# Optimization experiments

Measured on AMD Instinct MI355X. Metric: run time of the kernel, lower is better.

## Reference

```python
import jax, jax.numpy as jnp
import numpy as np

B, AT, NBR = 8, 96, 512
NG, NT = 25, 5            # n_gaussian_triple, n_theta
NANG = NG * NT            # 125, filternet input dim
NF = 128                  # n_filters
NB = 128                  # n_atom_basis


def ssp(x):
    # shifted softplus: ln(0.5*e^x + 0.5) = softplus(x) - ln(2)
    return jax.nn.softplus(x) - jnp.asarray(np.log(2.0), x.dtype)


def setup_inputs() -> dict:
    key = jax.random.key(0)
    ks = jax.random.split(key, 16)
    s = lambda fan_in: 1.0 / np.sqrt(fan_in)
    return {
        "x": jax.random.normal(ks[0], (B, AT, NB), jnp.float32),
        "triple_ijk": jax.random.uniform(ks[1], (B, AT, NBR, NANG), jnp.float32),
        "neighbors_j": jax.random.randint(ks[2], (B, AT, NBR), 0, AT, jnp.int32),
        "neighbors_k": jax.random.randint(ks[3], (B, AT, NBR), 0, AT, jnp.int32),
        "triple_mask": jnp.ones((B, AT, NBR), jnp.float32),
        # filter network (Dense ssp -> Dense linear)
        "W1": jax.random.normal(ks[4], (NANG, NF), jnp.float32) * s(NANG),
        "b1": jnp.zeros((NF,), jnp.float32),
        "W2": jax.random.normal(ks[5], (NF, NF), jnp.float32) * s(NF),
        "b2": jnp.zeros((NF,), jnp.float32),
        # cfconv in2f (no bias) and f2out (ssp activation)
        "Win": jax.random.normal(ks[6], (NB, NF), jnp.float32) * s(NB),
        "Wf2": jax.random.normal(ks[7], (NF, NB), jnp.float32) * s(NF),
        "bf2": jnp.zeros((NB,), jnp.float32),
        # final dense (linear) before residual
        "Wd": jax.random.normal(ks[8], (NB, NB), jnp.float32) * s(NB),
        "bd": jnp.zeros((NB,), jnp.float32),
    }


def _gather_atoms(y, nbh):
    # y: (B, At, F); nbh: (B, At, Nbr) -> (B, At, Nbr, F)
    b, at, nbr = nbh.shape
    idx = nbh.reshape(b, at * nbr, 1)
    return jnp.take_along_axis(y, idx, axis=1).reshape(b, at, nbr, y.shape[-1])


def reference(x, triple_ijk, neighbors_j, neighbors_k, triple_mask,
              W1, b1, W2, b2, Win, Wf2, bf2, Wd, bd):
    # filter network on angular/radial triple features -> (B, At, Nbr, NF)
    W_triple = ssp(triple_ijk @ W1 + b1) @ W2 + b2
    # in2f
    y = x @ Win                                  # (B, At, NF)
    y_j = _gather_atoms(y, neighbors_j)          # (B, At, Nbr, NF)
    y_k = _gather_atoms(y, neighbors_k)          # (B, At, Nbr, NF)
    # element-wise continuous-filter conv over triples, mask padded triples
    yt = y_j * y_k * W_triple * triple_mask[..., None]
    agg = jnp.sum(yt, axis=2)                    # sum-aggregate over triples
    v = ssp(agg @ Wf2 + bf2)                     # f2out with shifted softplus
    v = v @ Wd + bd                              # interaction dense
    return x + v                                 # residual
```

## Files before the change

### kernel.cpp

```cpp
#include <hip/hip_runtime.h>
#include <math.h>

#define B_    8
#define AT_   96
#define NBR_  512
#define NANG_ 125
#define NF_   128
#define NB_   128
#define TN    32
#define NCHUNK 2
#define CROWS (NBR_ / NCHUNK)
#define NTI   (CROWS / TN)
#define YSTB  40

typedef __attribute__((ext_vector_type(8))) short bf16x8;
typedef __attribute__((ext_vector_type(4))) float f32x4;
typedef __attribute__((ext_vector_type(4))) unsigned u32x4;

__device__ __forceinline__ short f2bf(float f) {
    union { float f; unsigned u; } x; x.f = f;
    return (short)((x.u + 0x8000u) >> 16);
}

__device__ __forceinline__ float bf2f(unsigned short u) {
    union { unsigned u; float f; } x; x.u = ((unsigned)u) << 16;
    return x.f;
}

__device__ __forceinline__ float sspf(float x) {
    float p = __builtin_amdgcn_exp2f(x * 1.44269504088896340736f);
    float l = __builtin_amdgcn_logf(1.0f + p);
    return 0.69314718055994530942f * l - 0.69314718055994530942f;
}

__device__ __forceinline__ unsigned cvtpk(float lo, float hi) {
    unsigned r;
    asm("v_cvt_pk_bf16_f32 %0, %1, %2" : "=v"(r) : "v"(lo), "v"(hi));
    return r;
}

__device__ __forceinline__ void block_sync_lds() {
    asm volatile("s_waitcnt lgkmcnt(0)" ::: "memory");
    __builtin_amdgcn_s_barrier();
    __builtin_amdgcn_sched_barrier(0);
}

__device__ __forceinline__ void load_tile(const float* __restrict__ tile,
                                          int row, int seg, float* v) {
    const float* s = tile + row * NANG_ + seg * 16;
    if (seg < 7) {
        #pragma unroll
        for (int j = 0; j < 16; j++) v[j] = s[j];
    } else {
        #pragma unroll
        for (int j = 0; j < 13; j++) v[j] = s[j];
        v[13] = 0.f; v[14] = 0.f; v[15] = 0.f;
    }
}

__device__ __forceinline__ void store_swz(short* dst, int row, int seg, const float* v) {
    unsigned r[8];
    #pragma unroll
    for (int i = 0; i < 8; i++) r[i] = cvtpk(v[2 * i], v[2 * i + 1]);
    const int swz = (row & 7) << 4;
    char* base = (char*)dst + row * 256;
    *(u32x4*)(base + ((seg * 32) ^ swz))      = (u32x4){r[0], r[1], r[2], r[3]};
    *(u32x4*)(base + ((seg * 32 + 16) ^ swz)) = (u32x4){r[4], r[5], r[6], r[7]};
}

__global__ __launch_bounds__(128) void prep_kernel(
    const float* __restrict__ x, const float* __restrict__ Win,
    const float* __restrict__ W1, const float* __restrict__ W2,
    float* __restrict__ y, short* __restrict__ w1p, short* __restrict__ w2p)
{
    __shared__ float xs[4][NB_];
    int blk = blockIdx.x, tid = threadIdx.x;
    if (blk < 192) {
        int row0 = blk * 4;
        #pragma unroll
        for (int r = 0; r < 4; r++) xs[r][tid] = x[(row0 + r) * NB_ + tid];
        __syncthreads();
        float a0 = 0.f, a1 = 0.f, a2 = 0.f, a3 = 0.f;
        #pragma unroll 8
        for (int k = 0; k < NB_; k++) {
            float w = Win[k * NF_ + tid];
            a0 = fmaf(xs[0][k], w, a0);
            a1 = fmaf(xs[1][k], w, a1);
            a2 = fmaf(xs[2][k], w, a2);
            a3 = fmaf(xs[3][k], w, a3);
        }
        y[(row0 + 0) * NF_ + tid] = a0;
        y[(row0 + 1) * NF_ + tid] = a1;
        y[(row0 + 2) * NF_ + tid] = a2;
        y[(row0 + 3) * NF_ + tid] = a3;
    } else {
        int t = (blk - 192) * 128 + tid;
        int j = t & 7, lane = (t >> 3) & 63, ks = (t >> 9) & 3, ct = t >> 11;
        int k = ks * 32 + (lane >> 4) * 8 + j;
        int n = ct * 16 + (lane & 15);
        w1p[t] = (k < NANG_) ? f2bf(W1[k * NF_ + n]) : (short)0;
        w2p[t] = f2bf(W2[k * NF_ + n]);
    }
}

__global__ __launch_bounds__(256, 3) void triple_partial(
    const float* __restrict__ trip,
    const int* __restrict__ nbj, const int* __restrict__ nbk,
    const float* __restrict__ maskg,
    const float* __restrict__ b1g, const float* __restrict__ b2g,
    const float* __restrict__ y, const short* __restrict__ w1p,
    const short* __restrict__ w2p, float* __restrict__ pagg)
{
    __shared__ short tileT[2][TN * 128];
    __shared__ short hs[2][TN * 128];
    __shared__ unsigned short yjkw[4][TN * YSTB];

    const int tid = threadIdx.x;
    const int wave = tid >> 6, lane = tid & 63;
    const int quad = lane >> 4, col = lane & 15;
    const int blk = blockIdx.x;
    const int bid = blk >> 1, c = blk & 1;
    const int b = bid / AT_;

    const float* tpc = trip + (long)bid * NBR_ * NANG_ + (long)c * CROWS * NANG_;
    const int nb_base = bid * NBR_ + c * CROWS;

    const int ct0 = 2 * wave, ct1 = 2 * wave + 1;
    const int f0 = ct0 * 16 + col, f1 = ct1 * 16 + col;
    const float bias1_0 = b1g[f0], bias1_1 = b1g[f1];
    const float bias2_0 = b2g[f0], bias2_1 = b2g[f1];

    const int trow = tid >> 3, tseg = tid & 7;
    const int row2 = lane >> 1, h = lane & 1;
    const int ycol = wave * 32 + h * 16;
    const int swzA = (col & 7) << 4;
    const int quad16 = quad * 16;

    bf16x8 w1f0[4], w1f1[4];
    #pragma unroll
    for (int ks = 0; ks < 4; ks++) {
        w1f0[ks] = *(const bf16x8*)&w1p[(ct0 * 4 + ks) * 512 + lane * 8];
        w1f1[ks] = *(const bf16x8*)&w1p[(ct1 * 4 + ks) * 512 + lane * 8];
    }

    int jn = nbj[nb_base + row2], kn = nbk[nb_base + row2];
    float mcur = maskg[nb_base + row2];
    f32x4 gj0, gj1, gj2, gj3, gk0, gk1, gk2, gk3;
    {
        const float* yj = y + (b * AT_ + jn) * NF_ + ycol;
        const float* yk = y + (b * AT_ + kn) * NF_ + ycol;
        gj0 = ((const f32x4*)yj)[0]; gj1 = ((const f32x4*)yj)[1];
        gj2 = ((const f32x4*)yj)[2]; gj3 = ((const f32x4*)yj)[3];
        gk0 = ((const f32x4*)yk)[0]; gk1 = ((const f32x4*)yk)[1];
        gk2 = ((const f32x4*)yk)[2]; gk3 = ((const f32x4*)yk)[3];
    }
    jn = nbj[nb_base + TN + row2];
    kn = nbk[nb_base + TN + row2];
    float mn = maskg[nb_base + TN + row2];

    float v[16];
    load_tile(tpc, trow, tseg, v);
    store_swz(&tileT[0][0], trow, tseg, v);
    block_sync_lds();

    float accw0 = 0.f, accw1 = 0.f;
    int cur = 0;

    for (int nt = 0; nt < NTI; nt++) {
        if (nt + 1 < NTI)
            load_tile(tpc + (nt + 1) * (TN * NANG_), trow, tseg, v);

        const char* tbA = (const char*)&tileT[cur][0] + col * 256;
        const char* tbB = (const char*)&tileT[cur][0] + (16 + col) * 256;
        f32x4 d00 = {0,0,0,0}, d01 = {0,0,0,0}, d10 = {0,0,0,0}, d11 = {0,0,0,0};
        #pragma unroll
        for (int ks = 0; ks < 4; ks++) {
            const int off = (ks * 64 + quad16) ^ swzA;
            bf16x8 a0 = *(const bf16x8*)(tbA + off);
            bf16x8 a1 = *(const bf16x8*)(tbB + off);
            d00 = __builtin_amdgcn_mfma_f32_16x16x32_bf16(a0, w1f0[ks], d00, 0, 0, 0);
            d01 = __builtin_amdgcn_mfma_f32_16x16x32_bf16(a0, w1f1[ks], d01, 0, 0, 0);
            d10 = __builtin_amdgcn_mfma_f32_16x16x32_bf16(a1, w1f0[ks], d10, 0, 0, 0);
            d11 = __builtin_amdgcn_mfma_f32_16x16x32_bf16(a1, w1f1[ks], d11, 0, 0, 0);
        }

        {
            f32x4 p0 = gj0 * gk0 * mcur, p1 = gj1 * gk1 * mcur;
            f32x4 p2 = gj2 * gk2 * mcur, p3 = gj3 * gk3 * mcur;
            unsigned y0 = cvtpk(p0.x, p0.y), y1 = cvtpk(p0.z, p0.w);
            unsigned y2 = cvtpk(p1.x, p1.y), y3 = cvtpk(p1.z, p1.w);
            unsigned y4 = cvtpk(p2.x, p2.y), y5 = cvtpk(p2.z, p2.w);
            unsigned y6 = cvtpk(p3.x, p3.y), y7 = cvtpk(p3.z, p3.w);
            unsigned short* d = &yjkw[wave][row2 * YSTB + h * 16];
            *(u32x4*)(d)     = (u32x4){y0, y1, y2, y3};
            *(u32x4*)(d + 8) = (u32x4){y4, y5, y6, y7};
        }
        {
            char* hw = (char*)&hs[cur][0];
            #pragma unroll
            for (int r = 0; r < 4; r++) {
                int row0 = quad * 4 + r, row1 = row0 + 16;
                int s0 = (row0 & 7) << 4;
                *(short*)(hw + row0 * 256 + ((2 * f0) ^ s0)) = f2bf(sspf(d00[r] + bias1_0));
                *(short*)(hw + row0 * 256 + ((2 * f1) ^ s0)) = f2bf(sspf(d01[r] + bias1_1));
                *(short*)(hw + row1 * 256 + ((2 * f0) ^ s0)) = f2bf(sspf(d10[r] + bias1_0));
                *(short*)(hw + row1 * 256 + ((2 * f1) ^ s0)) = f2bf(sspf(d11[r] + bias1_1));
            }
        }
        bf16x8 w2f0[4], w2f1[4];
        #pragma unroll
        for (int ks = 0; ks < 4; ks++) {
            w2f0[ks] = *(const bf16x8*)&w2p[(ct0 * 4 + ks) * 512 + lane * 8];
            w2f1[ks] = *(const bf16x8*)&w2p[(ct1 * 4 + ks) * 512 + lane * 8];
        }
        if (nt + 1 < NTI)
            store_swz(&tileT[cur ^ 1][0], trow, tseg, v);

        block_sync_lds();

        const char* hbA = (const char*)&hs[cur][0] + col * 256;
        const char* hbB = (const char*)&hs[cur][0] + (16 + col) * 256;
        f32x4 e00 = {0,0,0,0}, e01 = {0,0,0,0}, e10 = {0,0,0,0}, e11 = {0,0,0,0};
        #pragma unroll
        for (int ks = 0; ks < 4; ks++) {
            const int off = (ks * 64 + quad16) ^ swzA;
            bf16x8 a0 = *(const bf16x8*)(hbA + off);
            bf16x8 a1 = *(const bf16x8*)(hbB + off);
            e00 = __builtin_amdgcn_mfma_f32_16x16x32_bf16(a0, w2f0[ks], e00, 0, 0, 0);
            e01 = __builtin_amdgcn_mfma_f32_16x16x32_bf16(a0, w2f1[ks], e01, 0, 0, 0);
            e10 = __builtin_amdgcn_mfma_f32_16x16x32_bf16(a1, w2f0[ks], e10, 0, 0, 0);
            e11 = __builtin_amdgcn_mfma_f32_16x16x32_bf16(a1, w2f1[ks], e11, 0, 0, 0);
        }
        const unsigned short* yw = &yjkw[wave][0];
        #pragma unroll
        for (int r = 0; r < 4; r++) {
            int row0 = quad * 4 + r, row1 = row0 + 16;
            accw0 += (e00[r] + bias2_0) * bf2f(yw[row0 * YSTB + col]);
            accw1 += (e01[r] + bias2_1) * bf2f(yw[row0 * YSTB + col + 16]);
            accw0 += (e10[r] + bias2_0) * bf2f(yw[row1 * YSTB + col]);
            accw1 += (e11[r] + bias2_1) * bf2f(yw[row1 * YSTB + col + 16]);
        }

        if (nt + 1 < NTI) {
            const float* yj = y + (b * AT_ + jn) * NF_ + ycol;
            const float* yk = y + (b * AT_ + kn) * NF_ + ycol;
            gj0 = ((const f32x4*)yj)[0]; gj1 = ((const f32x4*)yj)[1];
            gj2 = ((const f32x4*)yj)[2]; gj3 = ((const f32x4*)yj)[3];
            gk0 = ((const f32x4*)yk)[0]; gk1 = ((const f32x4*)yk)[1];
            gk2 = ((const f32x4*)yk)[2]; gk3 = ((const f32x4*)yk)[3];
            mcur = mn;
            if (nt + 2 < NTI) {
                jn = nbj[nb_base + (nt + 2) * TN + row2];
                kn = nbk[nb_base + (nt + 2) * TN + row2];
                mn = maskg[nb_base + (nt + 2) * TN + row2];
            }
        }
        cur ^= 1;
    }

    accw0 += __shfl_xor(accw0, 16, 64);
    accw0 += __shfl_xor(accw0, 32, 64);
    accw1 += __shfl_xor(accw1, 16, 64);
    accw1 += __shfl_xor(accw1, 32, 64);
    if (quad == 0) {
        pagg[blk * NF_ + f0] = accw0;
        pagg[blk * NF_ + f1] = accw1;
    }
}

__global__ __launch_bounds__(128) void finish_kernel(
    const float* __restrict__ x, const float* __restrict__ pagg,
    const float* __restrict__ Wf2, const float* __restrict__ bf2,
    const float* __restrict__ Wd, const float* __restrict__ bd,
    float* __restrict__ out)
{
    __shared__ float aggs[NF_];
    __shared__ float t1s[NF_];
    int bid = blockIdx.x, f = threadIdx.x;
    float a = pagg[(bid * 2 + 0) * NF_ + f] + pagg[(bid * 2 + 1) * NF_ + f];
    aggs[f] = a;
    __syncthreads();
    float acc = 0.f;
    #pragma unroll 8
    for (int k = 0; k < NF_; k++) acc = fmaf(aggs[k], Wf2[k * NB_ + f], acc);
    t1s[f] = sspf(acc + bf2[f]);
    __syncthreads();
    acc = 0.f;
    #pragma unroll 8
    for (int k = 0; k < NB_; k++) acc = fmaf(t1s[k], Wd[k * NB_ + f], acc);
    out[bid * NB_ + f] = x[bid * NB_ + f] + acc + bd[f];
}

extern "C" void kernel_launch(void* const* d_in, const int* in_sizes, int n_in,
                              void* d_out, int out_size, void* d_ws, size_t ws_size,
                              hipStream_t stream) {
    const float* x    = (const float*)d_in[0];
    const float* trip = (const float*)d_in[1];
    const int*   nbj  = (const int*)d_in[2];
    const int*   nbk  = (const int*)d_in[3];
    const float* mask = (const float*)d_in[4];
    const float* W1   = (const float*)d_in[5];
    const float* b1   = (const float*)d_in[6];
    const float* W2   = (const float*)d_in[7];
    const float* b2   = (const float*)d_in[8];
    const float* Win  = (const float*)d_in[9];
    const float* Wf2  = (const float*)d_in[10];
    const float* bf2  = (const float*)d_in[11];
    const float* Wd   = (const float*)d_in[12];
    const float* bd   = (const float*)d_in[13];
    float* out = (float*)d_out;

    char* ws = (char*)d_ws;
    float* y    = (float*)ws;
    short* w1p  = (short*)(ws + 393216);
    short* w2p  = (short*)(ws + 393216 + 32768);
    float* pagg = (float*)(ws + 393216 + 65536);

    prep_kernel<<<320, 128, 0, stream>>>(x, Win, W1, W2, y, w1p, w2p);
    triple_partial<<<B_ * AT_ * NCHUNK, 256, 0, stream>>>(trip, nbj, nbk, mask,
        b1, b2, y, w1p, w2p, pagg);
    finish_kernel<<<B_ * AT_, 128, 0, stream>>>(x, pagg, Wf2, bf2, Wd, bd, out);
}
```

Measured before the change: 358.4 us.

## Split triples into four chunks, single-buffer LDS, and raise occupancy to four waves

Each atom's neighbor rows are now split across four blocks instead of two, and the finish kernel sums four partials. The tile and hidden LDS buffers drop from double to single buffering, and the neighbor gathers move from a two-step-ahead prefetch to the start of the current iteration. This cuts LDS and register use so the waves_per_eu(4,4) target can be met and more blocks run concurrently. In exchange it adds a second barrier per iteration and loses some overlap of global loads with MFMA work.

```diff
diff --git a/kernel.cpp b/kernel.cpp
--- a/kernel.cpp
+++ b/kernel.cpp
@@ -8,7 +8,7 @@
 #define NF_   128
 #define NB_   128
 #define TN    32
-#define NCHUNK 2
+#define NCHUNK 4
 #define CROWS (NBR_ / NCHUNK)
 #define NTI   (CROWS / TN)
 #define YSTB  40
@@ -103,7 +103,8 @@
     }
 }
 
-__global__ __launch_bounds__(256, 3) void triple_partial(
+__global__ __launch_bounds__(256) __attribute__((amdgpu_waves_per_eu(4, 4)))
+void triple_partial(
     const float* __restrict__ trip,
     const int* __restrict__ nbj, const int* __restrict__ nbk,
     const float* __restrict__ maskg,
@@ -111,15 +112,15 @@
     const float* __restrict__ y, const short* __restrict__ w1p,
     const short* __restrict__ w2p, float* __restrict__ pagg)
 {
-    __shared__ short tileT[2][TN * 128];
-    __shared__ short hs[2][TN * 128];
+    __shared__ short tileT[TN * 128];
+    __shared__ short hs[TN * 128];
     __shared__ unsigned short yjkw[4][TN * YSTB];
 
     const int tid = threadIdx.x;
     const int wave = tid >> 6, lane = tid & 63;
     const int quad = lane >> 4, col = lane & 15;
     const int blk = blockIdx.x;
-    const int bid = blk >> 1, c = blk & 1;
+    const int bid = blk >> 2, c = blk & 3;
     const int b = bid / AT_;
 
     const float* tpc = trip + (long)bid * NBR_ * NANG_ + (long)c * CROWS * NANG_;
@@ -143,35 +144,36 @@
         w1f1[ks] = *(const bf16x8*)&w1p[(ct1 * 4 + ks) * 512 + lane * 8];
     }
 
-    int jn = nbj[nb_base + row2], kn = nbk[nb_base + row2];
-    float mcur = maskg[nb_base + row2];
-    f32x4 gj0, gj1, gj2, gj3, gk0, gk1, gk2, gk3;
-    {
-        const float* yj = y + (b * AT_ + jn) * NF_ + ycol;
-        const float* yk = y + (b * AT_ + kn) * NF_ + ycol;
-        gj0 = ((const f32x4*)yj)[0]; gj1 = ((const f32x4*)yj)[1];
-        gj2 = ((const f32x4*)yj)[2]; gj3 = ((const f32x4*)yj)[3];
-        gk0 = ((const f32x4*)yk)[0]; gk1 = ((const f32x4*)yk)[1];
-        gk2 = ((const f32x4*)yk)[2]; gk3 = ((const f32x4*)yk)[3];
-    }
-    jn = nbj[nb_base + TN + row2];
-    kn = nbk[nb_base + TN + row2];
-    float mn = maskg[nb_base + TN + row2];
+    int jn = nbj[nb_base + row2];
+    int kn = nbk[nb_base + row2];
+    float mn = maskg[nb_base + row2];
 
     float v[16];
     load_tile(tpc, trow, tseg, v);
-    store_swz(&tileT[0][0], trow, tseg, v);
+    store_swz(&tileT[0], trow, tseg, v);
     block_sync_lds();
 
     float accw0 = 0.f, accw1 = 0.f;
-    int cur = 0;
 
     for (int nt = 0; nt < NTI; nt++) {
         if (nt + 1 < NTI)
             load_tile(tpc + (nt + 1) * (TN * NANG_), trow, tseg, v);
 
-        const char* tbA = (const char*)&tileT[cur][0] + col * 256;
-        const char* tbB = (const char*)&tileT[cur][0] + (16 + col) * 256;
+        const float* yj = y + (b * AT_ + jn) * NF_ + ycol;
+        const float* yk = y + (b * AT_ + kn) * NF_ + ycol;
+        f32x4 j0 = ((const f32x4*)yj)[0], j1 = ((const f32x4*)yj)[1];
+        f32x4 j2 = ((const f32x4*)yj)[2], j3 = ((const f32x4*)yj)[3];
+        f32x4 k0 = ((const f32x4*)yk)[0], k1 = ((const f32x4*)yk)[1];
+        f32x4 k2 = ((const f32x4*)yk)[2], k3 = ((const f32x4*)yk)[3];
+        const float mc = mn;
+        if (nt + 1 < NTI) {
+            jn = nbj[nb_base + (nt + 1) * TN + row2];
+            kn = nbk[nb_base + (nt + 1) * TN + row2];
+            mn = maskg[nb_base + (nt + 1) * TN + row2];
+        }
+
+        const char* tbA = (const char*)&tileT[0] + col * 256;
+        const char* tbB = (const char*)&tileT[0] + (16 + col) * 256;
         f32x4 d00 = {0,0,0,0}, d01 = {0,0,0,0}, d10 = {0,0,0,0}, d11 = {0,0,0,0};
         #pragma unroll
         for (int ks = 0; ks < 4; ks++) {
@@ -185,8 +187,8 @@
         }
 
         {
-            f32x4 p0 = gj0 * gk0 * mcur, p1 = gj1 * gk1 * mcur;
-            f32x4 p2 = gj2 * gk2 * mcur, p3 = gj3 * gk3 * mcur;
+            f32x4 p0 = j0 * k0 * mc, p1 = j1 * k1 * mc;
+            f32x4 p2 = j2 * k2 * mc, p3 = j3 * k3 * mc;
             unsigned y0 = cvtpk(p0.x, p0.y), y1 = cvtpk(p0.z, p0.w);
             unsigned y2 = cvtpk(p1.x, p1.y), y3 = cvtpk(p1.z, p1.w);
             unsigned y4 = cvtpk(p2.x, p2.y), y5 = cvtpk(p2.z, p2.w);
@@ -196,7 +198,7 @@
             *(u32x4*)(d + 8) = (u32x4){y4, y5, y6, y7};
         }
         {
-            char* hw = (char*)&hs[cur][0];
+            char* hw = (char*)&hs[0];
             #pragma unroll
             for (int r = 0; r < 4; r++) {
                 int row0 = quad * 4 + r, row1 = row0 + 16;
@@ -207,19 +209,20 @@
                 *(short*)(hw + row1 * 256 + ((2 * f1) ^ s0)) = f2bf(sspf(d11[r] + bias1_1));
             }
         }
+        block_sync_lds();
+
+        if (nt + 1 < NTI)
+            store_swz(&tileT[0], trow, tseg, v);
+
         bf16x8 w2f0[4], w2f1[4];
         #pragma unroll
         for (int ks = 0; ks < 4; ks++) {
             w2f0[ks] = *(const bf16x8*)&w2p[(ct0 * 4 + ks) * 512 + lane * 8];
             w2f1[ks] = *(const bf16x8*)&w2p[(ct1 * 4 + ks) * 512 + lane * 8];
         }
-        if (nt + 1 < NTI)
-            store_swz(&tileT[cur ^ 1][0], trow, tseg, v);
-
-        block_sync_lds();
-
-        const char* hbA = (const char*)&hs[cur][0] + col * 256;
-        const char* hbB = (const char*)&hs[cur][0] + (16 + col) * 256;
+
+        const char* hbA = (const char*)&hs[0] + col * 256;
+        const char* hbB = (const char*)&hs[0] + (16 + col) * 256;
         f32x4 e00 = {0,0,0,0}, e01 = {0,0,0,0}, e10 = {0,0,0,0}, e11 = {0,0,0,0};
         #pragma unroll
         for (int ks = 0; ks < 4; ks++) {
@@ -240,22 +243,7 @@
             accw0 += (e10[r] + bias2_0) * bf2f(yw[row1 * YSTB + col]);
             accw1 += (e11[r] + bias2_1) * bf2f(yw[row1 * YSTB + col + 16]);
         }
-
-        if (nt + 1 < NTI) {
-            const float* yj = y + (b * AT_ + jn) * NF_ + ycol;
-            const float* yk = y + (b * AT_ + kn) * NF_ + ycol;
-            gj0 = ((const f32x4*)yj)[0]; gj1 = ((const f32x4*)yj)[1];
-            gj2 = ((const f32x4*)yj)[2]; gj3 = ((const f32x4*)yj)[3];
-            gk0 = ((const f32x4*)yk)[0]; gk1 = ((const f32x4*)yk)[1];
-            gk2 = ((const f32x4*)yk)[2]; gk3 = ((const f32x4*)yk)[3];
-            mcur = mn;
-            if (nt + 2 < NTI) {
-                jn = nbj[nb_base + (nt + 2) * TN + row2];
-                kn = nbk[nb_base + (nt + 2) * TN + row2];
-                mn = maskg[nb_base + (nt + 2) * TN + row2];
-            }
-        }
-        cur ^= 1;
+        block_sync_lds();
     }
 
     accw0 += __shfl_xor(accw0, 16, 64);
@@ -277,7 +265,8 @@
     __shared__ float aggs[NF_];
     __shared__ float t1s[NF_];
     int bid = blockIdx.x, f = threadIdx.x;
-    float a = pagg[(bid * 2 + 0) * NF_ + f] + pagg[(bid * 2 + 1) * NF_ + f];
+    float a = pagg[(bid * 4 + 0) * NF_ + f] + pagg[(bid * 4 + 1) * NF_ + f]
+            + pagg[(bid * 4 + 2) * NF_ + f] + pagg[(bid * 4 + 3) * NF_ + f];
     aggs[f] = a;
     __syncthreads();
     float acc = 0.f;
```

Result: slower. 417.9 us (+16.6%).
